# Performance work log

Hardware: AMD Instinct MI355X
Metric: run time of the kernel (lower is better)

The kernel has to match this reference:

```python
import jax, jax.numpy as jnp
import numpy as np
import math

D_MODEL = 1024
N_HEADS = 16
D_HEAD = 64
D_MLP = 4096
INIT_RANGE = 0.02
VAR_EPS = 1e-05
BATCH = 2
SEQ = 2048


def new_gelu(x):
    c = math.sqrt(2.0 / math.pi)
    return 0.5 * x * (1.0 + jnp.tanh(c * (x + 0.044715 * x ** 3)))


def layer_norm(x, w, b):
    mean = jnp.mean(x, axis=-1, keepdims=True)
    x = x - mean
    var = jnp.mean(x * x, axis=-1, keepdims=True)
    return x / jnp.sqrt(var + VAR_EPS) * w + b


def setup_inputs() -> dict:
    key = jax.random.key(0)
    ks = jax.random.split(key, 12)
    s = INIT_RANGE
    return {
        "resid": jax.random.normal(ks[0], (BATCH, SEQ, D_MODEL), jnp.float32),
        "w_q": s * jax.random.normal(ks[1], (N_HEADS, D_MODEL, D_HEAD), jnp.float32),
        "w_k": s * jax.random.normal(ks[2], (N_HEADS, D_MODEL, D_HEAD), jnp.float32),
        "w_v": s * jax.random.normal(ks[3], (N_HEADS, D_MODEL, D_HEAD), jnp.float32),
        "w_o": s * jax.random.normal(ks[4], (N_HEADS, D_HEAD, D_MODEL), jnp.float32),
        "ln1_w": s * jax.random.normal(ks[5], (D_MODEL,), jnp.float32),
        "ln1_b": jnp.zeros((D_MODEL,), jnp.float32),
        "ln2_w": s * jax.random.normal(ks[6], (D_MODEL,), jnp.float32),
        "ln2_b": jnp.zeros((D_MODEL,), jnp.float32),
        "w_in": s * jax.random.normal(ks[7], (D_MODEL, D_MLP), jnp.float32),
        "b_in": jnp.zeros((D_MLP,), jnp.float32),
        "w_out": s * jax.random.normal(ks[8], (D_MLP, D_MODEL), jnp.float32),
        "b_out": jnp.zeros((D_MODEL,), jnp.float32),
    }


def attention(x, w_q, w_k, w_v, w_o):
    # x: [b, s, d]; weights: [h, d, dh] / [h, dh, d]
    qs = jnp.einsum('bsd,hde->bhse', x, w_q)
    ks = jnp.einsum('bsd,hde->bhse', x, w_k)
    vs = jnp.einsum('bsd,hde->bhse', x, w_v)
    attn = jnp.einsum('bhqe,bhke->bhqk', qs, ks)  # [b, h, s, s]
    s = attn.shape[-1]
    causal = jnp.triu(jnp.ones((s, s), dtype=bool), k=1)
    attn = jnp.where(causal, -jnp.inf, attn)
    attn = jax.nn.softmax(attn / math.sqrt(D_HEAD), axis=-1)
    z = jnp.einsum('bhqk,bhke->bhqe', attn, vs)
    return jnp.einsum('bhse,hed->bsd', z, w_o)


def reference(resid, w_q, w_k, w_v, w_o, ln1_w, ln1_b, ln2_w, ln2_b, w_in, b_in, w_out, b_out):
    resid = resid + attention(layer_norm(resid, ln1_w, ln1_b), w_q, w_k, w_v, w_o)
    h = layer_norm(resid, ln2_w, ln2_b)
    h = new_gelu(jnp.einsum('bsd,dm->bsm', h, w_in) + b_in)
    resid = resid + jnp.einsum('bsm,md->bsd', h, w_out) + b_out
    return resid
```

## Files before the change

kernel.cpp:

```cpp
#include <hip/hip_runtime.h>

#define DEV static __device__ __forceinline__

typedef unsigned short u16;
typedef __attribute__((ext_vector_type(8))) __bf16 bf16x8;
typedef __attribute__((ext_vector_type(4))) float f32x4;

DEV float bf2f(u16 u) { union { unsigned int i; float f; } v; v.i = ((unsigned int)u) << 16; return v.f; }
DEV u16 f2bf(float f) {
  union { float f; unsigned int i; } v; v.f = f;
  unsigned int r = v.i + 0x7fffu + ((v.i >> 16) & 1u);
  return (u16)(r >> 16);
}

DEV float gelu_f(float x) {
  float u = 0.7978845608028654f * (x + 0.044715f * x * x * x);
  float e = __expf(2.f * u);
  float t = 1.f - 2.f / (e + 1.f);
  return 0.5f * x * (1.f + t);
}

DEV void async16(const u16* g, u16* l) {
  __builtin_amdgcn_global_load_lds(
      (const __attribute__((address_space(1))) unsigned int*)g,
      (__attribute__((address_space(3))) unsigned int*)l, 16, 0, 0);
}

__global__ __launch_bounds__(256) void transpose_all(
    const float* __restrict__ w_q, const float* __restrict__ w_k,
    const float* __restrict__ w_v, const float* __restrict__ w_o,
    const float* __restrict__ w_in, const float* __restrict__ w_out,
    u16* __restrict__ WQKVT, u16* __restrict__ WOT,
    u16* __restrict__ WINT, u16* __restrict__ WOUTT)
{
  int t = blockIdx.x;
  const float* src; u16* dst; int R, C, c0, r0;
  if (t < 3072) {
    int seg = t >> 10, tt = t & 1023;
    int z = tt >> 6, rem = tt & 63;
    const float* w = seg == 0 ? w_q : (seg == 1 ? w_k : w_v);
    src = w + z * 65536;
    dst = WQKVT + seg * 1048576 + z * 65536;
    R = 1024; C = 64;
    c0 = (rem >> 5) * 32; r0 = (rem & 31) * 32;
  } else if (t < 4096) {
    int tt = t - 3072;
    src = w_o; dst = WOT; R = 1024; C = 1024;
    c0 = (tt & 31) * 32; r0 = (tt >> 5) * 32;
  } else if (t < 8192) {
    int tt = t - 4096;
    src = w_in; dst = WINT; R = 1024; C = 4096;
    c0 = (tt & 127) * 32; r0 = (tt >> 7) * 32;
  } else {
    int tt = t - 8192;
    src = w_out; dst = WOUTT; R = 4096; C = 1024;
    c0 = (tt & 31) * 32; r0 = (tt >> 5) * 32;
  }
  __shared__ float tile[32][33];
  int tx = threadIdx.x & 31, ty = threadIdx.x >> 5;
#pragma unroll
  for (int i = 0; i < 32; i += 8)
    tile[ty + i][tx] = src[(size_t)(r0 + ty + i) * C + (c0 + tx)];
  __syncthreads();
#pragma unroll
  for (int i = 0; i < 32; i += 8)
    dst[(size_t)(c0 + ty + i) * R + (r0 + tx)] = f2bf(tile[tx][ty + i]);
}

__global__ __launch_bounds__(256) void ln_kernel(
    const float* __restrict__ x, const float* __restrict__ g,
    const float* __restrict__ b, u16* __restrict__ out)
{
  int row = blockIdx.x, tid = threadIdx.x;
  const float4 v = ((const float4*)(x + (size_t)row * 1024))[tid];
  float s = v.x + v.y + v.z + v.w;
  float ss = v.x * v.x + v.y * v.y + v.z * v.z + v.w * v.w;
#pragma unroll
  for (int m = 1; m < 64; m <<= 1) { s += __shfl_xor(s, m, 64); ss += __shfl_xor(ss, m, 64); }
  __shared__ float red[8];
  if ((tid & 63) == 0) { red[tid >> 6] = s; red[4 + (tid >> 6)] = ss; }
  __syncthreads();
  s = red[0] + red[1] + red[2] + red[3];
  ss = red[4] + red[5] + red[6] + red[7];
  float mean = s * (1.f / 1024.f);
  float var = ss * (1.f / 1024.f) - mean * mean;
  float rstd = rsqrtf(var + 1e-5f);
  float4 gv = ((const float4*)g)[tid];
  float4 bv = ((const float4*)b)[tid];
  u16* o = out + (size_t)row * 1024 + tid * 4;
  o[0] = f2bf((v.x - mean) * rstd * gv.x + bv.x);
  o[1] = f2bf((v.y - mean) * rstd * gv.y + bv.y);
  o[2] = f2bf((v.z - mean) * rstd * gv.z + bv.z);
  o[3] = f2bf((v.w - mean) * rstd * gv.w + bv.w);
}

template <int EPI, int BM, int BN>
__global__ __launch_bounds__(256) void gemm_bf16(
    const u16* __restrict__ A, const u16* __restrict__ Bt, int K, int N,
    const float* __restrict__ addv, const float* __restrict__ bias,
    float* __restrict__ outF, u16* __restrict__ o0, u16* __restrict__ o1,
    u16* __restrict__ o2)
{
  static_assert(BM == 128 && BN == 64, "vmcnt literal assumes 6 loads/wave/stage");
  constexpr int IM = BM / 32, IN = BN / 32;
  __shared__ u16 lA[2][BM * 64];
  __shared__ u16 lB[2][BN * 64];
  const int tid = threadIdx.x;
  const int lane = tid & 63, wave = tid >> 6;
  const int wm = wave >> 1, wn = wave & 1;
  const int quad = lane >> 4, l16 = lane & 15;

  const int nwg = gridDim.x * gridDim.y;
  int flat = blockIdx.x + gridDim.x * blockIdx.y;
  flat = (flat & 7) * (nwg >> 3) + (flat >> 3);
  const int bx = flat % gridDim.x;
  const int by = flat / gridDim.x;
  const int m0 = by * BM, n0 = bx * BN;

  f32x4 acc[IM][IN] = {};

  const int srow = lane >> 3;
  const int soff = ((lane & 7) ^ srow) << 3;

  auto stage = [&](int bsel, int kt) {
#pragma unroll
    for (int q = 0; q < BM / 32; ++q) {
      int rbase = wave * (BM / 4) + q * 8;
      async16(A + (size_t)(m0 + rbase + srow) * K + kt + soff, lA[bsel] + rbase * 64);
    }
#pragma unroll
    for (int q = 0; q < BN / 32; ++q) {
      int rbase = wave * (BN / 4) + q * 8;
      async16(Bt + (size_t)(n0 + rbase + srow) * K + kt + soff, lB[bsel] + rbase * 64);
    }
  };

  const int T = K >> 6;
  stage(0, 0);
  stage(1, 64);

  for (int t = 0; t < T; ++t) {
    if (t == T - 1)
      asm volatile("s_waitcnt vmcnt(0)" ::: "memory");
    else
      asm volatile("s_waitcnt vmcnt(6)" ::: "memory");
    __builtin_amdgcn_s_barrier();

    const u16* cA = lA[t & 1];
    const u16* cB = lB[t & 1];
#pragma unroll
    for (int kk = 0; kk < 2; ++kk) {
      bf16x8 af[IM], bfr[IN];
#pragma unroll
      for (int i = 0; i < IM; ++i) {
        int ar = wm * (BM / 2) + i * 16 + l16;
        af[i] = *(const bf16x8*)&cA[ar * 64 + ((((kk * 4) + quad) ^ (ar & 7)) << 3)];
      }
#pragma unroll
      for (int j = 0; j < IN; ++j) {
        int br = wn * (BN / 2) + j * 16 + l16;
        bfr[j] = *(const bf16x8*)&cB[br * 64 + ((((kk * 4) + quad) ^ (br & 7)) << 3)];
      }
#pragma unroll
      for (int i = 0; i < IM; ++i)
#pragma unroll
        for (int j = 0; j < IN; ++j)
          acc[i][j] = __builtin_amdgcn_mfma_f32_16x16x32_bf16(af[i], bfr[j], acc[i][j], 0, 0, 0);
    }

    if (t + 2 < T) {
      asm volatile("s_waitcnt lgkmcnt(0)" ::: "memory");
      __builtin_amdgcn_s_barrier();
      stage(t & 1, (t + 2) << 6);
    }
  }

#pragma unroll
  for (int i = 0; i < IM; ++i) {
    const int rowb = m0 + wm * (BM / 2) + i * 16 + quad * 4;
#pragma unroll
    for (int j = 0; j < IN; ++j) {
      const int col = n0 + wn * (BN / 2) + j * 16 + l16;
#pragma unroll
      for (int rr = 0; rr < 4; ++rr) {
        const int m = rowb + rr;
        const float v = acc[i][j][rr];
        if (EPI == 0) {
          int bb = m >> 11, s = m & 2047;
          int proj = col >> 10, hc = col & 1023, hh = hc >> 6, e = hc & 63;
          size_t bhh = (size_t)(bb * 16 + hh);
          if (proj == 0) o0[(bhh * 2048 + s) * 64 + e] = f2bf(v * 0.125f);
          else if (proj == 1) o1[(bhh * 2048 + s) * 64 + e] = f2bf(v);
          else o2[bhh * 131072 + (size_t)e * 2048 + s] = f2bf(v);
        } else if (EPI == 1) {
          size_t idx = (size_t)m * N + col;
          outF[idx] = v + addv[idx];
        } else if (EPI == 2) {
          o0[(size_t)m * N + col] = f2bf(gelu_f(v + bias[col]));
        } else {
          size_t idx = (size_t)m * N + col;
          outF[idx] = v + bias[col] + addv[idx];
        }
      }
    }
  }
}

__global__ __launch_bounds__(256) void attn_flash(
    const u16* __restrict__ Q, const u16* __restrict__ K,
    const u16* __restrict__ Vt, u16* __restrict__ Z)
{
  __shared__ u16 lK[2][64 * 64];
  __shared__ u16 lV[2][64 * 64];
  __shared__ u16 lP[4][16 * 64];

  const int tid = threadIdx.x;
  const int lane = tid & 63, wave = tid >> 6;
  const int quad = lane >> 4, l16 = lane & 15;

  const int flat = blockIdx.x;
  const int xcd = flat & 7, w = flat >> 3;
  const int bhid = xcd * 4 + (w >> 4);
  const int p = w & 15;
  const int b = bhid >> 4, h = bhid & 15;
  const size_t bh = (size_t)bhid;

  const int nA = 32 - p;
  const int q0A = (31 - p) * 64;
  const int q0B = p * 64;

  const int srow = lane >> 3;
  const int soff = ((lane & 7) ^ srow) << 3;

  u16* myP = lP[wave];

  auto stage = [&](int buf, int s) {
    int kt0 = (s < nA ? s : s - nA) * 64;
#pragma unroll
    for (int q = 0; q < 2; ++q) {
      int rbase = wave * 16 + q * 8;
      async16(K + (bh * 2048 + (size_t)(kt0 + rbase + srow)) * 64 + soff,
              lK[buf] + rbase * 64);
      async16(Vt + bh * 131072 + (size_t)(rbase + srow) * 2048 + kt0 + soff,
              lV[buf] + rbase * 64);
    }
  };

  stage(0, 0);

  f32x4 oacc[4] = {};
  float lrow[4] = {};
  int q0w = q0A + wave * 16;

  bf16x8 qf[2];
#pragma unroll
  for (int d = 0; d < 2; ++d)
    qf[d] = *(const bf16x8*)(Q + (bh * 2048 + (size_t)(q0w + l16)) * 64 + d * 32 + quad * 8);

  auto writeO = [&]() {
#pragma unroll
    for (int rr = 0; rr < 4; ++rr) {
      float l = lrow[rr];
#pragma unroll
      for (int msk = 1; msk < 16; msk <<= 1) l += __shfl_xor(l, msk, 64);
      lrow[rr] = 1.f / l;
    }
#pragma unroll
    for (int d = 0; d < 4; ++d)
#pragma unroll
      for (int rr = 0; rr < 4; ++rr) {
        int srowq = q0w + quad * 4 + rr;
        Z[((size_t)(b * 2048 + srowq)) * 1024 + h * 64 + d * 16 + l16] =
            f2bf(oacc[d][rr] * lrow[rr]);
      }
  };

  for (int s = 0; s < 33; ++s) {
    if (s == nA) {
      writeO();
#pragma unroll
      for (int d = 0; d < 4; ++d)
#pragma unroll
        for (int e = 0; e < 4; ++e) oacc[d][e] = 0.f;
#pragma unroll
      for (int rr = 0; rr < 4; ++rr) lrow[rr] = 0.f;
      q0w = q0B + wave * 16;
#pragma unroll
      for (int d = 0; d < 2; ++d)
        qf[d] = *(const bf16x8*)(Q + (bh * 2048 + (size_t)(q0w + l16)) * 64 + d * 32 + quad * 8);
    }

    __syncthreads();
    if (s < 32) stage((s + 1) & 1, s + 1);

    const u16* cK = lK[s & 1];
    const u16* cV = lV[s & 1];
    const int kt0 = (s < nA ? s : s - nA) * 64;

    bf16x8 kf[4][2];
#pragma unroll
    for (int j = 0; j < 4; ++j)
#pragma unroll
      for (int d = 0; d < 2; ++d) {
        int key = j * 16 + l16;
        kf[j][d] = *(const bf16x8*)(cK + key * 64 + (((d * 4 + quad) ^ (key & 7)) << 3));
      }
    f32x4 sv[4];
#pragma unroll
    for (int j = 0; j < 4; ++j) {
      f32x4 z = {};
      z = __builtin_amdgcn_mfma_f32_16x16x32_bf16(qf[0], kf[j][0], z, 0, 0, 0);
      z = __builtin_amdgcn_mfma_f32_16x16x32_bf16(qf[1], kf[j][1], z, 0, 0, 0);
      sv[j] = z;
    }

    const bool needMask = (kt0 + 63 > q0w);
#pragma unroll
    for (int rr = 0; rr < 4; ++rr) {
      int rowl = quad * 4 + rr;
      int rowg = q0w + rowl;
      u16* prow = myP + rowl * 64;
      float accl = lrow[rr];
#pragma unroll
      for (int j = 0; j < 4; ++j) {
        float pv = __expf(sv[j][rr]);
        if (needMask && (kt0 + j * 16 + l16 > rowg)) pv = 0.f;
        accl += pv;
        int chk = j * 2 + (l16 >> 3);
        prow[((chk ^ (rowl & 7)) << 3) + (l16 & 7)] = (u16)(__float_as_uint(pv) >> 16);
      }
      lrow[rr] = accl;
    }

#pragma unroll
    for (int ks = 0; ks < 2; ++ks) {
      int chk = ks * 4 + quad;
      bf16x8 pf, vf[4];
      pf = *(const bf16x8*)(myP + l16 * 64 + ((chk ^ (l16 & 7)) << 3));
#pragma unroll
      for (int d = 0; d < 4; ++d) {
        int dh = d * 16 + l16;
        vf[d] = *(const bf16x8*)(cV + dh * 64 + ((chk ^ (dh & 7)) << 3));
      }
#pragma unroll
      for (int d = 0; d < 4; ++d)
        oacc[d] = __builtin_amdgcn_mfma_f32_16x16x32_bf16(pf, vf[d], oacc[d], 0, 0, 0);
    }
  }

  writeO();
}

extern "C" void kernel_launch(void* const* d_in, const int* in_sizes, int n_in,
                              void* d_out, int out_size, void* d_ws, size_t ws_size,
                              hipStream_t stream) {
  const float* resid = (const float*)d_in[0];
  const float* w_q  = (const float*)d_in[1];
  const float* w_k  = (const float*)d_in[2];
  const float* w_v  = (const float*)d_in[3];
  const float* w_o  = (const float*)d_in[4];
  const float* ln1w = (const float*)d_in[5];
  const float* ln1b = (const float*)d_in[6];
  const float* ln2w = (const float*)d_in[7];
  const float* ln2b = (const float*)d_in[8];
  const float* w_in = (const float*)d_in[9];
  const float* b_in = (const float*)d_in[10];
  const float* w_out= (const float*)d_in[11];
  const float* b_out= (const float*)d_in[12];
  float* out = (float*)d_out;

  const size_t MB = 1u << 20;
  char* ws = (char*)d_ws;
  u16* WQKVT = (u16*)(ws + 0);
  u16* WOT   = (u16*)(ws + 6 * MB);
  u16* WINT  = (u16*)(ws + 8 * MB);
  u16* WOUTT = (u16*)(ws + 16 * MB);
  u16* X1    = (u16*)(ws + 24 * MB);
  u16* Qb    = (u16*)(ws + 32 * MB);
  u16* Kb    = (u16*)(ws + 40 * MB);
  u16* Vb    = (u16*)(ws + 48 * MB);
  u16* Zb    = (u16*)(ws + 56 * MB);
  float* R2  = (float*)(ws + 64 * MB);
  u16* Hb    = (u16*)(ws + 80 * MB);
  u16* Gb    = (u16*)(ws + 24 * MB);

  transpose_all<<<dim3(12288), 256, 0, stream>>>(w_q, w_k, w_v, w_o, w_in, w_out,
                                                 WQKVT, WOT, WINT, WOUTT);
  ln_kernel<<<4096, 256, 0, stream>>>(resid, ln1w, ln1b, X1);
  gemm_bf16<0, 128, 64><<<dim3(48, 32), 256, 0, stream>>>(X1, WQKVT, 1024, 3072, nullptr, nullptr, nullptr, Qb, Kb, Vb);
  attn_flash<<<dim3(512), 256, 0, stream>>>(Qb, Kb, Vb, Zb);
  gemm_bf16<1, 128, 64><<<dim3(16, 32), 256, 0, stream>>>(Zb, WOT, 1024, 1024, resid, nullptr, R2, nullptr, nullptr, nullptr);
  ln_kernel<<<4096, 256, 0, stream>>>(R2, ln2w, ln2b, Hb);
  gemm_bf16<2, 128, 64><<<dim3(64, 32), 256, 0, stream>>>(Hb, WINT, 1024, 4096, nullptr, b_in, nullptr, Gb, nullptr, nullptr);
  gemm_bf16<3, 128, 64><<<dim3(16, 32), 256, 0, stream>>>(Gb, WOUTT, 4096, 1024, R2, b_out, out, nullptr, nullptr, nullptr);
}
```

Before: 360.5 us.

## Add 256x256-tile 8-wave phased GEMM for QKV and MLP-in projections

Introduces a new bf16 GEMM kernel using 256x256 block tiles with 8 waves (512 threads). Each K-step is split into four MFMA phases that interleave LDS fragment reads, async global-to-LDS staging of the next tile, barriers and s_setprio around the MFMA bursts. It replaces the 128x64 GEMM for the QKV projection and the MLP up-projection. The aim is more operand reuse per LDS byte and better overlap of loads with matrix math. In exchange the grid shrinks to 192 and 256 workgroups, which may underfill the 256 CUs, and register pressure rises.

Result: no change. 359.3 us (-0.3%).

```diff
diff --git a/kernel.cpp b/kernel.cpp
--- a/kernel.cpp
+++ b/kernel.cpp
@@ -94,6 +94,123 @@
   o[3] = f2bf((v.w - mean) * rstd * gv.w + bv.w);
 }
 
+#define GP_PHASE(MH, NH, RDA, BREG, RDB, BUF, STG_T, DOVM)                     \
+  {                                                                            \
+    const u16* cA = lA[BUF];                                                   \
+    const u16* cB = lB[BUF];                                                   \
+    if (RDA) {                                                                 \
+      _Pragma("unroll") for (int kk = 0; kk < 2; ++kk)                         \
+      _Pragma("unroll") for (int i = 0; i < 4; ++i) {                          \
+        int ar = wm * 128 + (MH) * 64 + i * 16 + l16;                          \
+        af[kk][i] = *(const bf16x8*)&cA[ar * 64 +                              \
+            (((kk * 4 + quad) ^ (ar & 7)) << 3)];                              \
+      }                                                                        \
+    }                                                                          \
+    if (RDB) {                                                                 \
+      _Pragma("unroll") for (int kk = 0; kk < 2; ++kk)                         \
+      _Pragma("unroll") for (int j = 0; j < 2; ++j) {                          \
+        int br = wn * 64 + (NH) * 32 + j * 16 + l16;                           \
+        BREG[kk][j] = *(const bf16x8*)&cB[br * 64 +                            \
+            (((kk * 4 + quad) ^ (br & 7)) << 3)];                              \
+      }                                                                        \
+    }                                                                          \
+    if ((STG_T) >= 0) {                                                        \
+      stageH(0, 0, STG_T); stageH(1, 0, STG_T);                                \
+      stageH(0, 1, STG_T); stageH(1, 1, STG_T);                                \
+    }                                                                          \
+    __builtin_amdgcn_s_barrier();                                              \
+    asm volatile("s_waitcnt lgkmcnt(0)" ::: "memory");                         \
+    __builtin_amdgcn_sched_barrier(0);                                         \
+    __builtin_amdgcn_s_setprio(1);                                             \
+    _Pragma("unroll") for (int kk = 0; kk < 2; ++kk)                           \
+    _Pragma("unroll") for (int i = 0; i < 4; ++i)                              \
+    _Pragma("unroll") for (int j = 0; j < 2; ++j)                              \
+      acc[(MH) * 4 + i][(NH) * 2 + j] =                                        \
+          __builtin_amdgcn_mfma_f32_16x16x32_bf16(                             \
+              af[kk][i], BREG[kk][j], acc[(MH) * 4 + i][(NH) * 2 + j], 0, 0, 0); \
+    __builtin_amdgcn_s_setprio(0);                                             \
+    if (DOVM) asm volatile("s_waitcnt vmcnt(0)" ::: "memory");                 \
+    __builtin_amdgcn_s_barrier();                                              \
+  }
+
+template <int EPI, int KI>
+__global__ __launch_bounds__(512, 2) void gemm_8ph(
+    const u16* __restrict__ A, const u16* __restrict__ Bt, int N,
+    const float* __restrict__ bias,
+    u16* __restrict__ o0, u16* __restrict__ o1, u16* __restrict__ o2)
+{
+  constexpr int NT = KI / 64;
+  __shared__ u16 lA[2][256 * 64];
+  __shared__ u16 lB[2][256 * 64];
+  const int tid = threadIdx.x;
+  const int lane = tid & 63, wave = tid >> 6;
+  const int wm = wave >> 2, wn = wave & 3;
+  const int quad = lane >> 4, l16 = lane & 15;
+
+  const int nwg = gridDim.x * gridDim.y;
+  int flat = blockIdx.x + gridDim.x * blockIdx.y;
+  flat = (flat & 7) * (nwg >> 3) + (flat >> 3);
+  const int bx = flat % gridDim.x, by = flat / gridDim.x;
+  const int m0 = by * 256, n0 = bx * 256;
+
+  const int srow = lane >> 3;
+  const int soff = ((lane & 7) ^ srow) << 3;
+
+  auto stageH = [&](int op, int hh, int t) {
+    int buf = t & 1;
+    int kt = (t & (NT - 1)) << 6;
+    u16* dst = (op ? lB[buf] : lA[buf]) + hh * (128 * 64) + wave * (16 * 64);
+    const u16* src = (op ? Bt : A) +
+        (size_t)((op ? n0 : m0) + hh * 128 + wave * 16 + srow) * KI + kt + soff;
+#pragma unroll
+    for (int q = 0; q < 2; ++q)
+      async16(src + (size_t)q * 8 * KI, dst + q * (8 * 64));
+  };
+
+  f32x4 acc[8][4] = {};
+  bf16x8 af[2][4], b0r[2][2], b1r[2][2];
+
+  stageH(0, 0, 0); stageH(1, 0, 0); stageH(0, 1, 0); stageH(1, 1, 0);
+  asm volatile("s_waitcnt vmcnt(0)" ::: "memory");
+  __builtin_amdgcn_s_barrier();
+
+  for (int it = 0; it < NT / 2; ++it) {
+    const int t1 = 2 * it + 1, t2 = 2 * it + 2;
+    GP_PHASE(0, 0, 1, b0r, 1, 0, t1, 0)
+    GP_PHASE(0, 1, 0, b1r, 1, 0, -1, 0)
+    GP_PHASE(1, 1, 1, b1r, 0, 0, -1, 0)
+    GP_PHASE(1, 0, 0, b0r, 0, 0, -1, 1)
+    GP_PHASE(0, 0, 1, b0r, 1, 1, t2, 0)
+    GP_PHASE(0, 1, 0, b1r, 1, 1, -1, 0)
+    GP_PHASE(1, 1, 1, b1r, 0, 1, -1, 0)
+    GP_PHASE(1, 0, 0, b0r, 0, 1, -1, 1)
+  }
+
+#pragma unroll
+  for (int mi = 0; mi < 8; ++mi) {
+    const int m = m0 + wm * 128 + mi * 16 + quad * 4;
+#pragma unroll
+    for (int nj = 0; nj < 4; ++nj) {
+      const int col = n0 + wn * 64 + nj * 16 + l16;
+#pragma unroll
+      for (int rr = 0; rr < 4; ++rr) {
+        const int mm = m + rr;
+        const float v = acc[mi][nj][rr];
+        if (EPI == 0) {
+          int bb = mm >> 11, s = mm & 2047;
+          int proj = col >> 10, hc = col & 1023, hh2 = hc >> 6, e = hc & 63;
+          size_t bhh = (size_t)(bb * 16 + hh2);
+          if (proj == 0) o0[(bhh * 2048 + s) * 64 + e] = f2bf(v * 0.125f);
+          else if (proj == 1) o1[(bhh * 2048 + s) * 64 + e] = f2bf(v);
+          else o2[bhh * 131072 + (size_t)e * 2048 + s] = f2bf(v);
+        } else {
+          o0[(size_t)mm * N + col] = f2bf(gelu_f(v + bias[col]));
+        }
+      }
+    }
+  }
+}
+
 template <int EPI, int BM, int BN>
 __global__ __launch_bounds__(256) void gemm_bf16(
     const u16* __restrict__ A, const u16* __restrict__ Bt, int K, int N,
@@ -387,10 +504,10 @@
   transpose_all<<<dim3(12288), 256, 0, stream>>>(w_q, w_k, w_v, w_o, w_in, w_out,
                                                  WQKVT, WOT, WINT, WOUTT);
   ln_kernel<<<4096, 256, 0, stream>>>(resid, ln1w, ln1b, X1);
-  gemm_bf16<0, 128, 64><<<dim3(48, 32), 256, 0, stream>>>(X1, WQKVT, 1024, 3072, nullptr, nullptr, nullptr, Qb, Kb, Vb);
+  gemm_8ph<0, 1024><<<dim3(12, 16), 512, 0, stream>>>(X1, WQKVT, 3072, nullptr, Qb, Kb, Vb);
   attn_flash<<<dim3(512), 256, 0, stream>>>(Qb, Kb, Vb, Zb);
   gemm_bf16<1, 128, 64><<<dim3(16, 32), 256, 0, stream>>>(Zb, WOT, 1024, 1024, resid, nullptr, R2, nullptr, nullptr, nullptr);
   ln_kernel<<<4096, 256, 0, stream>>>(R2, ln2w, ln2b, Hb);
-  gemm_bf16<2, 128, 64><<<dim3(64, 32), 256, 0, stream>>>(Hb, WINT, 1024, 4096, nullptr, b_in, nullptr, Gb, nullptr, nullptr);
+  gemm_8ph<2, 1024><<<dim3(16, 16), 512, 0, stream>>>(Hb, WINT, 4096, b_in, Gb, nullptr, nullptr);
   gemm_bf16<3, 128, 64><<<dim3(16, 32), 256, 0, stream>>>(Gb, WOUTT, 4096, 1024, R2, b_out, out, nullptr, nullptr, nullptr);
 }
```
